# Kernel tuning notes

Measured on AMD Instinct MI355X. Metric: run time of the kernel, lower is better.

Reference implementation:

```python
import jax, jax.numpy as jnp
import numpy as np

SIGMA_AGG = 0.5
NUM_SEG = 33  # labels in [0, 32]; 0 = background


def setup_inputs() -> dict:
    key = jax.random.key(0)
    k1, k2, k3, k4, k5 = jax.random.split(key, 5)
    B, C, H, W = 16, 4, 736, 736
    return {
        "pred_similarities": jax.random.normal(k1, (B, C, H, W), dtype=jnp.float32),
        "regions_mask": jax.random.uniform(k2, (B, 1, H, W), dtype=jnp.float32),
        "kernels_mask": jax.random.uniform(k3, (B, 1, H, W), dtype=jnp.float32),
        "text_mask_ndi_labels": jax.random.randint(k4, (B, 1, H, W), 0, NUM_SEG, dtype=jnp.int32),
        "kernel_mask_ndi_labels": jax.random.randint(k5, (B, 1, H, W), 0, NUM_SEG, dtype=jnp.int32),
    }


def _per_batch(pred, rmask, kmask, rlab, klab):
    # pred: [C, N]; rmask/kmask: [N]; rlab/klab: [N] int
    # Per-kernel-label sum of kernels_mask, scattered back; 0 where label==0.
    ksum = jax.ops.segment_sum(kmask, klab, num_segments=NUM_SEG)            # [S]
    kcard = jnp.where(klab > 0, ksum[klab], 0.0)                              # [N]
    # Per-kernel-label sum of pred_similarities per channel.
    psum = jax.ops.segment_sum(pred.T, klab, num_segments=NUM_SEG)            # [S, C]
    Gk = jnp.where(klab[None, :] > 0, psum[klab].T, 0.0)                      # [C, N]
    # Region cardinality: faithful to source, it sums kernels_mask (not regions_mask)
    # over region labels.
    rsum = jax.ops.segment_sum(kmask, rlab, num_segments=NUM_SEG)             # [S]
    rcard = jnp.where(rlab > 0, rsum[rlab], 0.0)                              # [N]
    return kcard, Gk, rcard


def reference(pred_similarities, regions_mask, kernels_mask,
              text_mask_ndi_labels, kernel_mask_ndi_labels):
    B, C, H, W = pred_similarities.shape
    N = H * W
    pred = pred_similarities.reshape(B, C, N)
    rmask = regions_mask.reshape(B, N)
    kmask = kernels_mask.reshape(B, N)
    rlab = text_mask_ndi_labels.reshape(B, N)
    klab = kernel_mask_ndi_labels.reshape(B, N)

    kcard, Gk, rcard = jax.vmap(_per_batch)(pred, rmask, kmask, rlab, klab)
    # kcard/rcard: [B, N], Gk: [B, C, N]

    Gk = Gk / (kcard[:, None, :] + 1.0)
    Fp = pred * rmask[:, None, :]
    norm = jnp.sqrt(jnp.sum((Fp - Gk) ** 2, axis=1))                          # [B, N]
    d = jnp.maximum(norm - SIGMA_AGG, 0.0)
    D_p_K = jnp.log(d ** 2 + 1.0) / (rcard + 1.0)
    # Faithful to source bug: num_kernel is the LAST batch's max kernel label.
    num_kernel = klab[-1].max().astype(D_p_K.dtype)
    L_agg = (D_p_K / num_kernel).sum()
    return L_agg
```

## Files before the change

kernel.cpp:

```cpp
#include <hip/hip_runtime.h>


constexpr int NSEG = 33;
constexpr int NCH  = 4;
constexpr int WS_PER_B = NSEG * (NCH + 2);
constexpr float SIGMA_AGG = 0.5f;
constexpr float QSCALE = 32768.0f;
constexpr float QINV   = 1.0f / 32768.0f;

constexpr int NUMK_OFF = 16 * WS_PER_B;
constexpr int PART_OFF = 3200;

__global__ __launch_bounds__(256) void seg_sums_kernel(
    const float* __restrict__ pred, const float* __restrict__ kmask,
    const int* __restrict__ rlab, const int* __restrict__ klab,
    int* __restrict__ ws, int* __restrict__ numk_out,
    int N, int lastB)
{
    const int b = blockIdx.y;
    __shared__ int s_acc[WS_PER_B];
    __shared__ int s_maxk;
    for (int j = threadIdx.x; j < WS_PER_B; j += blockDim.x) s_acc[j] = 0;
    if (threadIdx.x == 0) s_maxk = 0;
    __syncthreads();

    const size_t bN = (size_t)b * N;
    const int Nv = N >> 2;
    const float4* __restrict__ predv = (const float4*)(pred + (size_t)b * NCH * N);
    const float4* __restrict__ kmv   = (const float4*)(kmask + bN);
    const int4*   __restrict__ rlv   = (const int4*)(rlab + bN);
    const int4*   __restrict__ klv   = (const int4*)(klab + bN);

    int mk = 0;
    for (int i = blockIdx.x * blockDim.x + threadIdx.x; i < Nv;
         i += gridDim.x * blockDim.x) {
        float4 km = kmv[i];
        int4   kl = klv[i];
        int4   rl = rlv[i];
        float4 p0 = predv[0 * Nv + i];
        float4 p1 = predv[1 * Nv + i];
        float4 p2 = predv[2 * Nv + i];
        float4 p3 = predv[3 * Nv + i];

        #define PIX(sfx) do {                                                 \
            int kl_ = kl.sfx, rl_ = rl.sfx;                                   \
            int kq = __float2int_rn(km.sfx * QSCALE);                         \
            atomicAdd(&s_acc[kl_], kq);                                       \
            atomicAdd(&s_acc[NSEG + rl_], kq);                                \
            atomicAdd(&s_acc[2 * NSEG + 0 * NSEG + kl_],                      \
                      __float2int_rn(p0.sfx * QSCALE));                       \
            atomicAdd(&s_acc[2 * NSEG + 1 * NSEG + kl_],                      \
                      __float2int_rn(p1.sfx * QSCALE));                       \
            atomicAdd(&s_acc[2 * NSEG + 2 * NSEG + kl_],                      \
                      __float2int_rn(p2.sfx * QSCALE));                       \
            atomicAdd(&s_acc[2 * NSEG + 3 * NSEG + kl_],                      \
                      __float2int_rn(p3.sfx * QSCALE));                       \
            mk = max(mk, kl_);                                                \
        } while (0)
        PIX(x); PIX(y); PIX(z); PIX(w);
        #undef PIX
    }
    __syncthreads();

    int* wsb = ws + b * WS_PER_B;
    for (int j = threadIdx.x; j < WS_PER_B; j += blockDim.x)
        atomicAdd(&wsb[j], s_acc[j]);

    if (b == lastB) {
        atomicMax(&s_maxk, mk);
        __syncthreads();
        if (threadIdx.x == 0) atomicMax(numk_out, s_maxk);
    }
}

__global__ __launch_bounds__(256) void loss_kernel(
    const float* __restrict__ pred, const float* __restrict__ rmask,
    const int* __restrict__ rlab, const int* __restrict__ klab,
    const int* __restrict__ ws, float* __restrict__ partials, int N)
{
    const int b = blockIdx.y;
    __shared__ float s_gk[NCH * NSEG];
    __shared__ float s_rinv[NSEG];
    __shared__ float s_part[4];
    const int* wsb = ws + b * WS_PER_B;
    for (int j = threadIdx.x; j < NSEG; j += blockDim.x) {
        float rs = (float)wsb[NSEG + j] * QINV;
        s_rinv[j] = (j > 0) ? 1.0f / (rs + 1.0f) : 1.0f;
    }
    for (int j = threadIdx.x; j < NCH * NSEG; j += blockDim.x) {
        int s = j % NSEG;
        float ks = (float)wsb[s] * QINV;
        float ps = (float)wsb[2 * NSEG + j] * QINV;
        s_gk[j] = (s > 0) ? ps / (ks + 1.0f) : 0.0f;
    }
    __syncthreads();

    const size_t bN = (size_t)b * N;
    const int Nv = N >> 2;
    const float4* __restrict__ predv = (const float4*)(pred + (size_t)b * NCH * N);
    const float4* __restrict__ rmv   = (const float4*)(rmask + bN);
    const int4*   __restrict__ rlv   = (const int4*)(rlab + bN);
    const int4*   __restrict__ klv   = (const int4*)(klab + bN);

    float acc = 0.0f;
    for (int i = blockIdx.x * blockDim.x + threadIdx.x; i < Nv;
         i += gridDim.x * blockDim.x) {
        float4 rm = rmv[i];
        int4   kl = klv[i];
        int4   rl = rlv[i];
        float4 p0 = predv[0 * Nv + i];
        float4 p1 = predv[1 * Nv + i];
        float4 p2 = predv[2 * Nv + i];
        float4 p3 = predv[3 * Nv + i];

        #define PIX(sfx) do {                                        \
            int kl_ = kl.sfx, rl_ = rl.sfx; float rm_ = rm.sfx;      \
            float d0 = fmaf(p0.sfx, rm_, -s_gk[0 * NSEG + kl_]);     \
            float d1 = fmaf(p1.sfx, rm_, -s_gk[1 * NSEG + kl_]);     \
            float d2 = fmaf(p2.sfx, rm_, -s_gk[2 * NSEG + kl_]);     \
            float d3 = fmaf(p3.sfx, rm_, -s_gk[3 * NSEG + kl_]);     \
            float ss = d0*d0 + d1*d1 + d2*d2 + d3*d3;                \
            float nrm = sqrtf(ss);                                   \
            float dd = fmaxf(nrm - SIGMA_AGG, 0.0f);                 \
            acc += __logf(fmaf(dd, dd, 1.0f)) * s_rinv[rl_];         \
        } while (0)
        PIX(x); PIX(y); PIX(z); PIX(w);
        #undef PIX
    }

    for (int off = 32; off > 0; off >>= 1)
        acc += __shfl_down(acc, off);
    const int lane = threadIdx.x & 63;
    const int wid  = threadIdx.x >> 6;
    if (lane == 0) s_part[wid] = acc;
    __syncthreads();
    if (threadIdx.x == 0)
        partials[blockIdx.y * gridDim.x + blockIdx.x] =
            s_part[0] + s_part[1] + s_part[2] + s_part[3];
}

__global__ __launch_bounds__(256) void finalize_kernel(
    const float* __restrict__ partials, const int* __restrict__ numk,
    float* __restrict__ out, int nPart)
{
    __shared__ float s_part[4];
    float a = 0.0f;
    for (int i = threadIdx.x; i < nPart; i += blockDim.x) a += partials[i];
    for (int off = 32; off > 0; off >>= 1)
        a += __shfl_down(a, off);
    if ((threadIdx.x & 63) == 0) s_part[threadIdx.x >> 6] = a;
    __syncthreads();
    if (threadIdx.x == 0)
        out[0] = (s_part[0] + s_part[1] + s_part[2] + s_part[3]) / (float)(*numk);
}

extern "C" void kernel_launch(void* const* d_in, const int* in_sizes, int n_in,
                              void* d_out, int out_size, void* d_ws, size_t ws_size,
                              hipStream_t stream)
{
    const float* pred  = (const float*)d_in[0];
    const float* rmask = (const float*)d_in[1];
    const float* kmask = (const float*)d_in[2];
    const int*   rlab  = (const int*)d_in[3];
    const int*   klab  = (const int*)d_in[4];
    float* out = (float*)d_out;

    const int B = 16;
    const int N = in_sizes[1] / B;

    int* wsi = (int*)d_ws;
    int* numk = wsi + NUMK_OFF;
    float* partials = (float*)(wsi + PART_OFF);

    hipMemsetAsync(d_ws, 0, (size_t)(NUMK_OFF + 1) * sizeof(int), stream);

    dim3 block(256);
    dim3 grid(256, B);
    seg_sums_kernel<<<grid, block, 0, stream>>>(pred, kmask, rlab, klab, wsi, numk, N, B - 1);
    loss_kernel<<<grid, block, 0, stream>>>(pred, rmask, rlab, klab, wsi, partials, N);
    finalize_kernel<<<dim3(1), block, 0, stream>>>(partials, numk, out, 256 * B);
}
```

Baseline: 327.5 us.

## Pack segment sums into 64-bit shared atomics and skip label-zero updates

The six 32-bit shared-memory atomics per pixel become two 64-bit packed atomics, one 32-bit atomic on kernel labels and one on region labels, with carry correction on unpack. Pixels whose label is zero (background) now skip their atomics, since those sums are never used. The loss kernel reads the per-segment centroid as a single float4 from shared memory instead of four scalar reads. Packed accumulation relies on the low 32-bit half never overflowing, and 64-bit LDS atomics may be slower than 32-bit ones.

```diff
diff --git a/kernel.cpp b/kernel.cpp
--- a/kernel.cpp
+++ b/kernel.cpp
@@ -2,31 +2,47 @@
 
 
 constexpr int NSEG = 33;
-constexpr int NCH  = 4;
-constexpr int WS_PER_B = NSEG * (NCH + 2);
 constexpr float SIGMA_AGG = 0.5f;
-constexpr float QSCALE = 32768.0f;
-constexpr float QINV   = 1.0f / 32768.0f;
-
-constexpr int NUMK_OFF = 16 * WS_PER_B;
-constexpr int PART_OFF = 3200;
+constexpr float QS = 32768.0f;
+constexpr float QI = 1.0f / 32768.0f;
+
+constexpr size_t OFF_B    = 4224;
+constexpr size_t OFF_C    = 8448;
+constexpr size_t OFF_D    = 10560;
+constexpr size_t OFF_NUMK = 12672;
+constexpr size_t OFF_PART = 12800;
+constexpr size_t ZERO_BYTES = 12676;
+
+__device__ inline unsigned long long pack2(int hi, int lo) {
+    return ((unsigned long long)(unsigned)hi << 32) + (unsigned long long)(long long)lo;
+}
+__device__ inline void unpack2(unsigned long long v, int& hi, int& lo) {
+    int l = (int)(unsigned)(v & 0xFFFFFFFFull);
+    int h = (int)(unsigned)(v >> 32);
+    lo = l;
+    hi = h + (l < 0 ? 1 : 0);
+}
 
 __global__ __launch_bounds__(256) void seg_sums_kernel(
     const float* __restrict__ pred, const float* __restrict__ kmask,
     const int* __restrict__ rlab, const int* __restrict__ klab,
-    int* __restrict__ ws, int* __restrict__ numk_out,
+    unsigned long long* __restrict__ wsA, unsigned long long* __restrict__ wsB,
+    int* __restrict__ wsC, int* __restrict__ wsD, int* __restrict__ numk_out,
     int N, int lastB)
 {
     const int b = blockIdx.y;
-    __shared__ int s_acc[WS_PER_B];
+    __shared__ unsigned long long sA[NSEG], sB[NSEG];
+    __shared__ int sC[NSEG], sD[NSEG];
     __shared__ int s_maxk;
-    for (int j = threadIdx.x; j < WS_PER_B; j += blockDim.x) s_acc[j] = 0;
+    for (int j = threadIdx.x; j < NSEG; j += blockDim.x) {
+        sA[j] = 0ull; sB[j] = 0ull; sC[j] = 0; sD[j] = 0;
+    }
     if (threadIdx.x == 0) s_maxk = 0;
     __syncthreads();
 
     const size_t bN = (size_t)b * N;
     const int Nv = N >> 2;
-    const float4* __restrict__ predv = (const float4*)(pred + (size_t)b * NCH * N);
+    const float4* __restrict__ predv = (const float4*)(pred + (size_t)b * 4 * N);
     const float4* __restrict__ kmv   = (const float4*)(kmask + bN);
     const int4*   __restrict__ rlv   = (const int4*)(rlab + bN);
     const int4*   __restrict__ klv   = (const int4*)(klab + bN);
@@ -44,27 +60,29 @@
 
         #define PIX(sfx) do {                                                 \
             int kl_ = kl.sfx, rl_ = rl.sfx;                                   \
-            int kq = __float2int_rn(km.sfx * QSCALE);                         \
-            atomicAdd(&s_acc[kl_], kq);                                       \
-            atomicAdd(&s_acc[NSEG + rl_], kq);                                \
-            atomicAdd(&s_acc[2 * NSEG + 0 * NSEG + kl_],                      \
-                      __float2int_rn(p0.sfx * QSCALE));                       \
-            atomicAdd(&s_acc[2 * NSEG + 1 * NSEG + kl_],                      \
-                      __float2int_rn(p1.sfx * QSCALE));                       \
-            atomicAdd(&s_acc[2 * NSEG + 2 * NSEG + kl_],                      \
-                      __float2int_rn(p2.sfx * QSCALE));                       \
-            atomicAdd(&s_acc[2 * NSEG + 3 * NSEG + kl_],                      \
-                      __float2int_rn(p3.sfx * QSCALE));                       \
+            int qk = __float2int_rn(km.sfx * QS);                             \
             mk = max(mk, kl_);                                                \
+            if (kl_ != 0) {                                                   \
+                atomicAdd(&sA[kl_],                                           \
+                          pack2(__float2int_rn(p0.sfx * QS), qk));            \
+                atomicAdd(&sB[kl_],                                           \
+                          pack2(__float2int_rn(p2.sfx * QS),                  \
+                                __float2int_rn(p1.sfx * QS)));                \
+                atomicAdd(&sC[kl_], __float2int_rn(p3.sfx * QS));             \
+            }                                                                 \
+            if (rl_ != 0) atomicAdd(&sD[rl_], qk);                            \
         } while (0)
         PIX(x); PIX(y); PIX(z); PIX(w);
         #undef PIX
     }
     __syncthreads();
 
-    int* wsb = ws + b * WS_PER_B;
-    for (int j = threadIdx.x; j < WS_PER_B; j += blockDim.x)
-        atomicAdd(&wsb[j], s_acc[j]);
+    for (int j = threadIdx.x; j < NSEG; j += blockDim.x) {
+        if (sA[j]) atomicAdd(&wsA[b * NSEG + j], sA[j]);
+        if (sB[j]) atomicAdd(&wsB[b * NSEG + j], sB[j]);
+        if (sC[j]) atomicAdd(&wsC[b * NSEG + j], sC[j]);
+        if (sD[j]) atomicAdd(&wsD[b * NSEG + j], sD[j]);
+    }
 
     if (b == lastB) {
         atomicMax(&s_maxk, mk);
@@ -76,28 +94,31 @@
 __global__ __launch_bounds__(256) void loss_kernel(
     const float* __restrict__ pred, const float* __restrict__ rmask,
     const int* __restrict__ rlab, const int* __restrict__ klab,
-    const int* __restrict__ ws, float* __restrict__ partials, int N)
+    const unsigned long long* __restrict__ wsA,
+    const unsigned long long* __restrict__ wsB,
+    const int* __restrict__ wsC, const int* __restrict__ wsD,
+    float* __restrict__ partials, int N)
 {
     const int b = blockIdx.y;
-    __shared__ float s_gk[NCH * NSEG];
-    __shared__ float s_rinv[NSEG];
-    __shared__ float s_part[4];
-    const int* wsb = ws + b * WS_PER_B;
+    __shared__ float4 s_gk4[NSEG];
+    __shared__ float  s_rinv[NSEG];
+    __shared__ float  s_part[4];
     for (int j = threadIdx.x; j < NSEG; j += blockDim.x) {
-        float rs = (float)wsb[NSEG + j] * QINV;
+        int p0q, ksq, p2q, p1q;
+        unpack2(wsA[b * NSEG + j], p0q, ksq);
+        unpack2(wsB[b * NSEG + j], p2q, p1q);
+        float ks = (float)ksq * QI;
+        float inv = (j > 0) ? 1.0f / (ks + 1.0f) : 0.0f;
+        s_gk4[j] = make_float4((float)p0q * QI * inv, (float)p1q * QI * inv,
+                               (float)p2q * QI * inv, (float)wsC[b * NSEG + j] * QI * inv);
+        float rs = (float)wsD[b * NSEG + j] * QI;
         s_rinv[j] = (j > 0) ? 1.0f / (rs + 1.0f) : 1.0f;
-    }
-    for (int j = threadIdx.x; j < NCH * NSEG; j += blockDim.x) {
-        int s = j % NSEG;
-        float ks = (float)wsb[s] * QINV;
-        float ps = (float)wsb[2 * NSEG + j] * QINV;
-        s_gk[j] = (s > 0) ? ps / (ks + 1.0f) : 0.0f;
     }
     __syncthreads();
 
     const size_t bN = (size_t)b * N;
     const int Nv = N >> 2;
-    const float4* __restrict__ predv = (const float4*)(pred + (size_t)b * NCH * N);
+    const float4* __restrict__ predv = (const float4*)(pred + (size_t)b * 4 * N);
     const float4* __restrict__ rmv   = (const float4*)(rmask + bN);
     const int4*   __restrict__ rlv   = (const int4*)(rlab + bN);
     const int4*   __restrict__ klv   = (const int4*)(klab + bN);
@@ -114,15 +135,14 @@
         float4 p3 = predv[3 * Nv + i];
 
         #define PIX(sfx) do {                                        \
-            int kl_ = kl.sfx, rl_ = rl.sfx; float rm_ = rm.sfx;      \
-            float d0 = fmaf(p0.sfx, rm_, -s_gk[0 * NSEG + kl_]);     \
-            float d1 = fmaf(p1.sfx, rm_, -s_gk[1 * NSEG + kl_]);     \
-            float d2 = fmaf(p2.sfx, rm_, -s_gk[2 * NSEG + kl_]);     \
-            float d3 = fmaf(p3.sfx, rm_, -s_gk[3 * NSEG + kl_]);     \
+            float4 g = s_gk4[kl.sfx]; float rm_ = rm.sfx;            \
+            float d0 = fmaf(p0.sfx, rm_, -g.x);                      \
+            float d1 = fmaf(p1.sfx, rm_, -g.y);                      \
+            float d2 = fmaf(p2.sfx, rm_, -g.z);                      \
+            float d3 = fmaf(p3.sfx, rm_, -g.w);                      \
             float ss = d0*d0 + d1*d1 + d2*d2 + d3*d3;                \
-            float nrm = sqrtf(ss);                                   \
-            float dd = fmaxf(nrm - SIGMA_AGG, 0.0f);                 \
-            acc += __logf(fmaf(dd, dd, 1.0f)) * s_rinv[rl_];         \
+            float dd = fmaxf(sqrtf(ss) - SIGMA_AGG, 0.0f);           \
+            acc += __logf(fmaf(dd, dd, 1.0f)) * s_rinv[rl.sfx];      \
         } while (0)
         PIX(x); PIX(y); PIX(z); PIX(w);
         #undef PIX
@@ -168,15 +188,21 @@
     const int B = 16;
     const int N = in_sizes[1] / B;
 
-    int* wsi = (int*)d_ws;
-    int* numk = wsi + NUMK_OFF;
-    float* partials = (float*)(wsi + PART_OFF);
-
-    hipMemsetAsync(d_ws, 0, (size_t)(NUMK_OFF + 1) * sizeof(int), stream);
+    char* wsc = (char*)d_ws;
+    unsigned long long* wsA = (unsigned long long*)wsc;
+    unsigned long long* wsB = (unsigned long long*)(wsc + OFF_B);
+    int*   wsC      = (int*)(wsc + OFF_C);
+    int*   wsD      = (int*)(wsc + OFF_D);
+    int*   numk     = (int*)(wsc + OFF_NUMK);
+    float* partials = (float*)(wsc + OFF_PART);
+
+    hipMemsetAsync(d_ws, 0, ZERO_BYTES, stream);
 
     dim3 block(256);
     dim3 grid(256, B);
-    seg_sums_kernel<<<grid, block, 0, stream>>>(pred, kmask, rlab, klab, wsi, numk, N, B - 1);
-    loss_kernel<<<grid, block, 0, stream>>>(pred, rmask, rlab, klab, wsi, partials, N);
+    seg_sums_kernel<<<grid, block, 0, stream>>>(pred, kmask, rlab, klab,
+                                                wsA, wsB, wsC, wsD, numk, N, B - 1);
+    loss_kernel<<<grid, block, 0, stream>>>(pred, rmask, rlab, klab,
+                                            wsA, wsB, wsC, wsD, partials, N);
     finalize_kernel<<<dim3(1), block, 0, stream>>>(partials, numk, out, 256 * B);
 }
```

Result: no change. 329.3 us (+0.6%).
